# Performance work log

Measured on AMD Instinct MI355X. Metric: run time of the kernel, lower is better.

The kernel has to match this reference:

```python
import math
import jax, jax.numpy as jnp
import numpy as np

B, T, E = 2, 2048, 2048
H, HKV = 16, 4
DH = E // H              # 128
ROT_DIM = DH             # rotary_pct = 1.0 -> 128
ROT_HALF = ROT_DIM // 2  # RotaryEmbedding is built with dim=ROT_DIM//2=64; only these dims rotate
MAX_SEQ = 2048


def _rope_tables():
    # theta = 10000 ** (-arange(0, dim, 2)/dim) with dim = ROT_HALF
    theta = 10000.0 ** (-jnp.arange(0, ROT_HALF, 2, dtype=jnp.float32) / ROT_HALF)  # [ROT_HALF//2]
    pos = jnp.arange(MAX_SEQ, dtype=jnp.float32)
    angles = pos[:, None] * theta[None, :]   # [MAX_SEQ, ROT_HALF//2]
    return jnp.cos(angles), jnp.sin(angles)


def _apply_rotary(q, k, start_pos):
    # q: [B,T,H,ROT_DIM], k: [B,T,HKV,ROT_DIM]; rotate only first ROT_HALF dims (interleaved pairs)
    cos, sin = _rope_tables()
    t = q.shape[1]
    cos = jax.lax.dynamic_slice_in_dim(cos, start_pos, t, axis=0)[None, :, None, :]
    sin = jax.lax.dynamic_slice_in_dim(sin, start_pos, t, axis=0)[None, :, None, :]

    def rot(a):
        a_rot, a_pass = a[..., :ROT_HALF], a[..., ROT_HALF:]
        x, y = a_rot[..., 0::2], a_rot[..., 1::2]
        rx = x * cos - y * sin
        ry = x * sin + y * cos
        rotated = jnp.stack([rx, ry], axis=-1).reshape(*a_rot.shape)
        return jnp.concatenate([rotated, a_pass], axis=-1)

    return rot(q), rot(k)


def setup_inputs() -> dict:
    key = jax.random.key(0)
    ks = jax.random.split(key, 9)
    s = 0.02  # weight scale for sane logits
    return {
        "x": jax.random.normal(ks[0], (B, T, E), dtype=jnp.float32),
        "Wq": jax.random.normal(ks[1], (E, H * DH), dtype=jnp.float32) * s,
        "bq": jax.random.normal(ks[2], (H * DH,), dtype=jnp.float32) * s,
        "Wk": jax.random.normal(ks[3], (E, HKV * DH), dtype=jnp.float32) * s,
        "bk": jax.random.normal(ks[4], (HKV * DH,), dtype=jnp.float32) * s,
        "Wv": jax.random.normal(ks[5], (E, HKV * DH), dtype=jnp.float32) * s,
        "bv": jax.random.normal(ks[6], (HKV * DH,), dtype=jnp.float32) * s,
        "Wo": jax.random.normal(ks[7], (E, E), dtype=jnp.float32) * s,
        "bo": jax.random.normal(ks[8], (E,), dtype=jnp.float32) * s,
        "start_pos": 0,
    }


def reference(x, Wq, bq, Wk, bk, Wv, bv, Wo, bo, start_pos):
    b, t, _ = x.shape
    q = (x @ Wq + bq).reshape(b, t, H, DH)
    k = (x @ Wk + bk).reshape(b, t, HKV, DH)
    v = (x @ Wv + bv).reshape(b, t, HKV, DH)

    q, k = _apply_rotary(q, k, start_pos)

    group = H // HKV
    k = jnp.repeat(k, group, axis=2)  # [b,t,H,DH]
    v = jnp.repeat(v, group, axis=2)

    # scores: [b,H,t,t]
    scores = jnp.einsum("bqhd,bkhd->bhqk", q, k) / math.sqrt(DH)
    causal = jnp.tril(jnp.ones((t, t), dtype=bool))
    scores = jnp.where(causal[None, None], scores, -jnp.inf)
    probs = jax.nn.softmax(scores, axis=-1)

    out = jnp.einsum("bhqk,bkhd->bqhd", probs, v).reshape(b, t, H * DH)
    return out @ Wo + bo
```

## Files before the change

### kernel.cpp

```cpp
#include <hip/hip_runtime.h>

typedef __attribute__((ext_vector_type(8))) short short8;
typedef __attribute__((ext_vector_type(4))) float f32x4;
typedef __attribute__((ext_vector_type(16))) float f32x16;

#define DEVFN __device__ __forceinline__

DEVFN unsigned short f2bf(float f) {
  unsigned int u = __builtin_bit_cast(unsigned int, f);
  u += 0x7FFFu + ((u >> 16) & 1u);
  return (unsigned short)(u >> 16);
}
DEVFN float bf2f(unsigned int u) { return __builtin_bit_cast(float, u << 16); }

DEVFN unsigned int cvtpk_bf16(float lo, float hi) {
  unsigned int d;
  asm("v_cvt_pk_bf16_f32 %0, %1, %2" : "=v"(d) : "v"(lo), "v"(hi));
  return d;
}
DEVFN void plswap32(unsigned int& a, unsigned int& b) {
  asm("v_permlane32_swap_b32 %0, %1" : "+v"(a), "+v"(b));
}
DEVFN float bcast32(float v, int srclane) {
  int r = __builtin_amdgcn_ds_bpermute(srclane * 4, __builtin_bit_cast(int, v));
  return __builtin_bit_cast(float, r);
}


__global__ __launch_bounds__(256) void mk_tables(float* __restrict__ cost, float* __restrict__ sint) {
  int gid = blockIdx.x * 256 + threadIdx.x;
  int pos = gid >> 5, i = gid & 31;
  float theta = powf(10000.0f, -(float)(2 * i) / 64.0f);
  float ang = (float)pos * theta;
  cost[gid] = cosf(ang);
  sint[gid] = sinf(ang);
}

__global__ __launch_bounds__(256) void bias_cat_k(const float* __restrict__ bq, const float* __restrict__ bk,
                                                  const float* __restrict__ bv, float* __restrict__ out) {
  int i = blockIdx.x * 256 + threadIdx.x;
  float v;
  if (i < 2048) v = bq[i];
  else if (i < 2560) v = bk[i - 2048];
  else v = bv[i - 2560];
  out[i] = v;
}

__global__ __launch_bounds__(256) void convx(const float* __restrict__ x, unsigned short* __restrict__ xb) {
  int gid = blockIdx.x * 256 + threadIdx.x;
  const float4* xv = (const float4*)x;
  float4 a = xv[(size_t)gid * 2], b = xv[(size_t)gid * 2 + 1];
  short8 u;
  u[0] = (short)f2bf(a.x); u[1] = (short)f2bf(a.y); u[2] = (short)f2bf(a.z); u[3] = (short)f2bf(a.w);
  u[4] = (short)f2bf(b.x); u[5] = (short)f2bf(b.y); u[6] = (short)f2bf(b.z); u[7] = (short)f2bf(b.w);
  *(short8*)(xb + (size_t)gid * 8) = u;
}

__global__ __launch_bounds__(256) void transw(const float* __restrict__ W, unsigned short* __restrict__ Wt, int ncols) {
  __shared__ float lds[32][33];
  int n0 = blockIdx.x * 32, k0 = blockIdx.y * 32;
  int tx = threadIdx.x & 31, ty = threadIdx.x >> 5;
  #pragma unroll
  for (int i = 0; i < 4; i++) {
    int kr = ty + i * 8;
    lds[kr][tx] = W[(size_t)(k0 + kr) * ncols + n0 + tx];
  }
  __syncthreads();
  #pragma unroll
  for (int i = 0; i < 4; i++) {
    int nr = ty + i * 8;
    Wt[(size_t)(n0 + nr) * 2048 + k0 + tx] = f2bf(lds[tx][nr]);
  }
}

template<int NH>
__global__ __launch_bounds__(256) void rope_scatter(const unsigned short* __restrict__ QKV,
    const float* __restrict__ cost, const float* __restrict__ sint, const int* __restrict__ spp,
    unsigned short* __restrict__ dst, int colOff, float scale) {
  constexpr int LOG2NH = (NH == 16) ? 4 : 2;
  int gid = blockIdx.x * 256 + threadIdx.x;
  int j = gid & 63;
  int h = (gid >> 6) & (NH - 1);
  int m = gid >> (6 + LOG2NH);
  int t = m & 2047;
  int b = m >> 11;
  const unsigned short* src = QKV + (size_t)m * 3072 + colOff + h * 128 + 2 * j;
  unsigned int pair = *(const unsigned int*)src;
  float xv = bf2f(pair & 0xFFFFu), yv = bf2f(pair >> 16);
  float rx, ry;
  if (j < 32) {
    int pos = (spp[0] + t) & 2047;
    float c = cost[pos * 32 + j], s = sint[pos * 32 + j];
    rx = xv * c - yv * s;
    ry = xv * s + yv * c;
  } else { rx = xv; ry = yv; }
  rx *= scale; ry *= scale;
  int d0 = 2 * j;
  size_t off = (size_t)(b * NH + h) * 262144 + (t >> 5) * 4096 + (d0 >> 4) * 512
             + ((d0 >> 3) & 1) * 256 + (t & 31) * 8 + (d0 & 7);
  unsigned int outp = (unsigned int)f2bf(rx) | ((unsigned int)f2bf(ry) << 16);
  *(unsigned int*)(dst + off) = outp;
}

__global__ __launch_bounds__(256) void vtrans(const unsigned short* __restrict__ QKV, unsigned short* __restrict__ VF) {
  __shared__ __align__(16) unsigned short lds[64 * 128];
  int tid = threadIdx.x;
  int t0 = blockIdx.x * 64;
  int bk = blockIdx.y;
  const unsigned short* src = QKV + (size_t)(bk >> 2) * 2048 * 3072 + 2560 + (bk & 3) * 128;
  #pragma unroll
  for (int c = 0; c < 4; c++) {
    int idx = c * 256 + tid;
    int tr = idx >> 4, dc = idx & 15;
    short8 v = *(const short8*)(src + (size_t)(t0 + tr) * 3072 + dc * 8);
    *(short8*)((char*)lds + tr * 256 + 16 * (dc ^ (tr >> 3))) = v;
  }
  __syncthreads();
  unsigned short* dstb = VF + (size_t)bk * 262144;
  #pragma unroll
  for (int c2 = 0; c2 < 4; c2++) {
    int idx2 = c2 * 256 + tid;
    int tc = idx2 & 7, d = idx2 >> 3;
    short8 u;
    #pragma unroll
    for (int e = 0; e < 8; e++) {
      int t = 8 * tc + e;
      u[e] = *(const short*)((char*)lds + t * 256 + 16 * ((d >> 3) ^ tc) + (d & 7) * 2);
    }
    size_t off = (size_t)(t0 >> 6) * 8192 + ((d >> 5) * 4 + ((tc >> 1) & 3)) * 512
               + (tc & 1) * 256 + (d & 31) * 8;
    *(short8*)(dstb + off) = u;
  }
}

template<bool BF16OUT>
__global__ __launch_bounds__(256, 2) void gemm_bt(
    const unsigned short* __restrict__ A, const unsigned short* __restrict__ Bt,
    const float* __restrict__ bias, void* __restrict__ Cout, int M, int N, int K) {
  __shared__ __align__(16) unsigned short Asl[128 * 64];
  __shared__ __align__(16) unsigned short Bsl[128 * 64];
  int tid = threadIdx.x;
  int lane = tid & 63, w = tid >> 6;
  int wr = w >> 1, wc = w & 1;
  int m0 = blockIdx.y * 128, n0 = blockIdx.x * 128;

  f32x4 acc[4][4];
  #pragma unroll
  for (int i = 0; i < 4; i++)
    #pragma unroll
    for (int j = 0; j < 4; j++)
      #pragma unroll
      for (int r = 0; r < 4; r++) acc[i][j][r] = 0.f;

  int srow = w * 32 + (lane >> 3);
  int kc8 = (lane & 7) * 8;
  const unsigned short* Aptr = A + (size_t)(m0 + srow) * K + kc8;
  const unsigned short* Bptr = Bt + (size_t)(n0 + srow) * K + kc8;
  unsigned short* AslW = Asl + w * 4 * 512;
  unsigned short* BslW = Bsl + w * 4 * 512;

  for (int k0 = 0; k0 < K; k0 += 64) {
    __syncthreads();
    #pragma unroll
    for (int i = 0; i < 4; i++) {
      __builtin_amdgcn_global_load_lds(
        (const __attribute__((address_space(1))) unsigned int*)(Aptr + (size_t)i * 8 * K + k0),
        (__attribute__((address_space(3))) unsigned int*)(AslW + i * 512), 16, 0, 0);
      __builtin_amdgcn_global_load_lds(
        (const __attribute__((address_space(1))) unsigned int*)(Bptr + (size_t)i * 8 * K + k0),
        (__attribute__((address_space(3))) unsigned int*)(BslW + i * 512), 16, 0, 0);
    }
    __syncthreads();
    #pragma unroll
    for (int ks = 0; ks < 2; ks++) {
      short8 af[4], bfr[4];
      #pragma unroll
      for (int mi = 0; mi < 4; mi++)
        af[mi] = *(const short8*)(Asl + (wr * 64 + mi * 16 + (lane & 15)) * 64 + ks * 32 + (lane >> 4) * 8);
      #pragma unroll
      for (int ni = 0; ni < 4; ni++)
        bfr[ni] = *(const short8*)(Bsl + (wc * 64 + ni * 16 + (lane & 15)) * 64 + ks * 32 + (lane >> 4) * 8);
      #pragma unroll
      for (int mi = 0; mi < 4; mi++)
        #pragma unroll
        for (int ni = 0; ni < 4; ni++)
          acc[mi][ni] = __builtin_amdgcn_mfma_f32_16x16x32_bf16(af[mi], bfr[ni], acc[mi][ni], 0, 0, 0);
    }
  }
  int cl = lane & 15, rq = lane >> 4;
  #pragma unroll
  for (int mi = 0; mi < 4; mi++) {
    #pragma unroll
    for (int ni = 0; ni < 4; ni++) {
      int gn = n0 + wc * 64 + ni * 16 + cl;
      float bv = bias[gn];
      #pragma unroll
      for (int r = 0; r < 4; r++) {
        int gm = m0 + wr * 64 + mi * 16 + rq * 4 + r;
        float v = acc[mi][ni][r] + bv;
        if (BF16OUT) ((unsigned short*)Cout)[(size_t)gm * N + gn] = f2bf(v);
        else ((float*)Cout)[(size_t)gm * N + gn] = v;
      }
    }
  }
}

__global__ __launch_bounds__(512, 2) void attn_kernel(
    const unsigned short* __restrict__ QF, const unsigned short* __restrict__ KF,
    const unsigned short* __restrict__ VF, unsigned short* __restrict__ O) {
  const int tid = threadIdx.x;
  const int lane = tid & 63;
  const int w = tid >> 6;
  const int l31 = lane & 31;
  const int hf = lane >> 5;
  const int g = blockIdx.x & 7, j = blockIdx.x >> 3;
  const int b = g >> 2, kh = g & 3;
  const int h = kh * 4 + (j & 3);
  const int i4 = (j >> 2) * 4;
  const int qt = (w < 4) ? (i4 + w) : (67 - i4 - w);
  const int qw = qt * 32;
  const int nw = (qt >> 1) + 1;

  const unsigned short* qh  = QF + (size_t)(b * 16 + h) * 262144 + qt * 4096;
  const unsigned short* khp = KF + (size_t)(b * 4 + kh) * 262144;
  const unsigned short* vhp = VF + (size_t)(b * 4 + kh) * 262144;

  short8 qf[8];
  #pragma unroll
  for (int s = 0; s < 8; s++)
    qf[s] = *(const short8*)(qh + s * 512 + lane * 8);

  float m_r = -3.0e38f, l_r = 0.f;
  f32x16 oacc[4];
  #pragma unroll
  for (int dt = 0; dt < 4; dt++)
    #pragma unroll
    for (int r = 0; r < 16; r++) oacc[dt][r] = 0.f;

  for (int kt = 0; kt < nw; kt++) {
    const int kv0 = kt * 64;
    f32x16 sc[2];
    {
      short8 kf0[8];
      #pragma unroll
      for (int s = 0; s < 8; s++)
        kf0[s] = *(const short8*)(khp + (size_t)(2 * kt) * 4096 + s * 512 + lane * 8);
      #pragma unroll
      for (int r = 0; r < 16; r++) sc[0][r] = 0.f;
      #pragma unroll
      for (int s = 0; s < 8; s++)
        sc[0] = __builtin_amdgcn_mfma_f32_32x32x16_bf16(kf0[s], qf[s], sc[0], 0, 0, 0);
    }
    {
      short8 kf1[8];
      #pragma unroll
      for (int s = 0; s < 8; s++)
        kf1[s] = *(const short8*)(khp + (size_t)(2 * kt + 1) * 4096 + s * 512 + lane * 8);
      #pragma unroll
      for (int r = 0; r < 16; r++) sc[1][r] = 0.f;
      #pragma unroll
      for (int s = 0; s < 8; s++)
        sc[1] = __builtin_amdgcn_mfma_f32_32x32x16_bf16(kf1[s], qf[s], sc[1], 0, 0, 0);
    }
    short8 vf[4][4];
    #pragma unroll
    for (int dt = 0; dt < 4; dt++)
      #pragma unroll
      for (int ks = 0; ks < 4; ks++)
        vf[dt][ks] = *(const short8*)(vhp + (size_t)kt * 8192 + (dt * 4 + ks) * 512 + lane * 8);

    if (kv0 + 63 > qw) {
      #pragma unroll
      for (int ct = 0; ct < 2; ct++)
        #pragma unroll
        for (int r = 0; r < 16; r++) {
          int kg = kv0 + ct * 32 + (r & 3) + 8 * (r >> 2) + 4 * hf;
          if (kg > qw + l31) sc[ct][r] = -3.0e38f;
        }
    }
    float mx[16];
    #pragma unroll
    for (int r = 0; r < 16; r++) mx[r] = fmaxf(sc[0][r], sc[1][r]);
    #pragma unroll
    for (int s2 = 8; s2 >= 1; s2 >>= 1)
      #pragma unroll
      for (int i = 0; i < 8; i++) if (i < s2) mx[i] = fmaxf(mx[i], mx[i + s2]);
    float tm = fmaxf(mx[0], __shfl_xor(mx[0], 32));
    if (__any(tm > m_r + 8.0f)) {
      float mn = fmaxf(m_r, tm);
      float al = __builtin_amdgcn_exp2f(m_r - mn);
      m_r = mn;
      l_r *= al;
      #pragma unroll
      for (int r = 0; r < 16; r++) {
        float alr = bcast32(al, (r & 3) + 8 * (r >> 2) + 4 * hf);
        #pragma unroll
        for (int dt = 0; dt < 4; dt++) oacc[dt][r] *= alr;
      }
    }
    #pragma unroll
    for (int ct = 0; ct < 2; ct++)
      #pragma unroll
      for (int r = 0; r < 16; r++) sc[ct][r] = __builtin_amdgcn_exp2f(sc[ct][r] - m_r);
    float sm[16];
    #pragma unroll
    for (int r = 0; r < 16; r++) sm[r] = sc[0][r] + sc[1][r];
    #pragma unroll
    for (int s2 = 8; s2 >= 1; s2 >>= 1)
      #pragma unroll
      for (int i = 0; i < 8; i++) if (i < s2) sm[i] += sm[i + s2];
    l_r += sm[0];

    short8 pa[4];
    #pragma unroll
    for (int ks = 0; ks < 4; ks++) {
      const int ct = ks >> 1, kb = (ks & 1) * 8;
      unsigned int A0 = cvtpk_bf16(sc[ct][kb + 0], sc[ct][kb + 1]);
      unsigned int A1 = cvtpk_bf16(sc[ct][kb + 2], sc[ct][kb + 3]);
      unsigned int B0 = cvtpk_bf16(sc[ct][kb + 4], sc[ct][kb + 5]);
      unsigned int B1 = cvtpk_bf16(sc[ct][kb + 6], sc[ct][kb + 7]);
      plswap32(A0, B0);
      plswap32(A1, B1);
      union { unsigned int wds[4]; short8 s8; } u;
      u.wds[0] = A0; u.wds[1] = A1; u.wds[2] = B0; u.wds[3] = B1;
      pa[ks] = u.s8;
    }
    #pragma unroll
    for (int dt = 0; dt < 4; dt++)
      #pragma unroll
      for (int ks = 0; ks < 4; ks++)
        oacc[dt] = __builtin_amdgcn_mfma_f32_32x32x16_bf16(pa[ks], vf[dt][ks], oacc[dt], 0, 0, 0);
  }
  float invl = 1.0f / (l_r + __shfl_xor(l_r, 32));
  #pragma unroll
  for (int r = 0; r < 16; r++) {
    int rloc = (r & 3) + 8 * (r >> 2) + 4 * hf;
    float inv = bcast32(invl, rloc);
    int qg = qw + rloc;
    unsigned short* orow = O + ((size_t)(b * 2048 + qg)) * 2048 + h * 128;
    #pragma unroll
    for (int dt = 0; dt < 4; dt++)
      orow[dt * 32 + l31] = f2bf(oacc[dt][r] * inv);
  }
}

extern "C" void kernel_launch(void* const* d_in, const int* in_sizes, int n_in,
                              void* d_out, int out_size, void* d_ws, size_t ws_size,
                              hipStream_t stream) {
  (void)in_sizes; (void)n_in; (void)out_size; (void)ws_size;
  const float* x  = (const float*)d_in[0];
  const float* Wq = (const float*)d_in[1];
  const float* bq = (const float*)d_in[2];
  const float* Wk = (const float*)d_in[3];
  const float* bk = (const float*)d_in[4];
  const float* Wv = (const float*)d_in[5];
  const float* bv = (const float*)d_in[6];
  const float* Wo = (const float*)d_in[7];
  const float* bo = (const float*)d_in[8];
  const int*   sp = (const int*)d_in[9];

  char* ws = (char*)d_ws;
  unsigned short* xb    = (unsigned short*)ws;
  unsigned short* Wqkvt = (unsigned short*)(ws + 16777216);
  unsigned short* Wot   = (unsigned short*)(ws + 29360128);
  unsigned short* QKVb  = (unsigned short*)(ws + 37748736);
  float* cost           = (float*)(ws + 62914560);
  float* sint           = (float*)(ws + 63176704);
  float* bcat           = (float*)(ws + 63438848);

  unsigned short* Obuf = xb;
  unsigned short* QFr = (unsigned short*)d_out;
  unsigned short* KFr = (unsigned short*)((char*)d_out + 16777216);
  unsigned short* VFr = (unsigned short*)((char*)d_out + 20971520);

  mk_tables<<<256, 256, 0, stream>>>(cost, sint);
  bias_cat_k<<<12, 256, 0, stream>>>(bq, bk, bv, bcat);
  convx<<<4096, 256, 0, stream>>>(x, xb);
  transw<<<dim3(64, 64), 256, 0, stream>>>(Wq, Wqkvt, 2048);
  transw<<<dim3(16, 64), 256, 0, stream>>>(Wk, Wqkvt + (size_t)2048 * 2048, 512);
  transw<<<dim3(16, 64), 256, 0, stream>>>(Wv, Wqkvt + (size_t)2560 * 2048, 512);
  transw<<<dim3(64, 64), 256, 0, stream>>>(Wo, Wot, 2048);
  gemm_bt<true><<<dim3(24, 32), 256, 0, stream>>>(xb, Wqkvt, bcat, QKVb, 4096, 3072, 2048);
  rope_scatter<16><<<16384, 256, 0, stream>>>(QKVb, cost, sint, sp, QFr, 0, 0.12751743f);
  rope_scatter<4><<<4096, 256, 0, stream>>>(QKVb, cost, sint, sp, KFr, 2048, 1.0f);
  vtrans<<<dim3(32, 8), 256, 0, stream>>>(QKVb, VFr);
  attn_kernel<<<dim3(256), 512, 0, stream>>>(QFr, KFr, VFr, Obuf);
  gemm_bt<false><<<dim3(16, 32), 256, 0, stream>>>(Obuf, Wot, bo, (float*)d_out, 4096, 2048, 2048);
}
```

Before: 237.9 us.

## Split attention KV range across wave pairs with LDS merge of partial softmax

Each query tile is now handled by a pair of waves that each process half of the causal KV tiles. The partial output accumulators and the m/l statistics are combined through shared memory with a rescaled log-sum-exp merge. The grid doubles to 512 blocks, each covering 4 query tiles instead of 8, which gives more parallelism and shortens each wave's serial KV loop. The cost is 64KB of LDS per block, a block-wide barrier and extra merge work, and the launch bound now asks for 4 blocks per CU, which may cap register use.

```diff
diff --git a/kernel.cpp b/kernel.cpp
--- a/kernel.cpp
+++ b/kernel.cpp
@@ -205,21 +205,29 @@
   }
 }
 
-__global__ __launch_bounds__(512, 2) void attn_kernel(
+__global__ __launch_bounds__(512, 4) void attn_kernel(
     const unsigned short* __restrict__ QF, const unsigned short* __restrict__ KF,
     const unsigned short* __restrict__ VF, unsigned short* __restrict__ O) {
+  __shared__ float mbuf[4 * 4096];
+  __shared__ float mlb[4 * 128];
+
   const int tid = threadIdx.x;
   const int lane = tid & 63;
   const int w = tid >> 6;
+  const int p = w >> 1;
+  const int role = w & 1;
   const int l31 = lane & 31;
   const int hf = lane >> 5;
   const int g = blockIdx.x & 7, j = blockIdx.x >> 3;
   const int b = g >> 2, kh = g & 3;
   const int h = kh * 4 + (j & 3);
-  const int i4 = (j >> 2) * 4;
-  const int qt = (w < 4) ? (i4 + w) : (67 - i4 - w);
+  const int qg = j >> 2;
+  const int qt = (p < 2) ? (2 * qg + p) : (60 - 2 * qg + p);
   const int qw = qt * 32;
-  const int nw = (qt >> 1) + 1;
+  const int nt = (qt >> 1) + 1;
+  const int ntA = nt >> 1;
+  const int kt0 = role ? ntA : 0;
+  const int kt1 = role ? nt : ntA;
 
   const unsigned short* qh  = QF + (size_t)(b * 16 + h) * 262144 + qt * 4096;
   const unsigned short* khp = KF + (size_t)(b * 4 + kh) * 262144;
@@ -237,7 +245,7 @@
     #pragma unroll
     for (int r = 0; r < 16; r++) oacc[dt][r] = 0.f;
 
-  for (int kt = 0; kt < nw; kt++) {
+  for (int kt = kt0; kt < kt1; kt++) {
     const int kv0 = kt * 64;
     f32x16 sc[2];
     {
@@ -331,16 +339,41 @@
       for (int ks = 0; ks < 4; ks++)
         oacc[dt] = __builtin_amdgcn_mfma_f32_32x32x16_bf16(pa[ks], vf[dt][ks], oacc[dt], 0, 0, 0);
   }
-  float invl = 1.0f / (l_r + __shfl_xor(l_r, 32));
-  #pragma unroll
-  for (int r = 0; r < 16; r++) {
-    int rloc = (r & 3) + 8 * (r >> 2) + 4 * hf;
-    float inv = bcast32(invl, rloc);
-    int qg = qw + rloc;
-    unsigned short* orow = O + ((size_t)(b * 2048 + qg)) * 2048 + h * 128;
+
+  float lw = l_r + __shfl_xor(l_r, 32);
+  if (role) {
+    float* bp = mbuf + p * 4096;
     #pragma unroll
     for (int dt = 0; dt < 4; dt++)
-      orow[dt * 32 + l31] = f2bf(oacc[dt][r] * inv);
+      #pragma unroll
+      for (int r = 0; r < 16; r++)
+        bp[(dt * 16 + r) * 64 + lane] = oacc[dt][r];
+    mlb[p * 128 + lane] = m_r;
+    mlb[p * 128 + 64 + lane] = lw;
+  }
+  __syncthreads();
+  if (!role) {
+    const float* bp = mbuf + p * 4096;
+    float mB = mlb[p * 128 + lane];
+    float lB = mlb[p * 128 + 64 + lane];
+    float mm = fmaxf(m_r, mB);
+    float alA = __builtin_amdgcn_exp2f(m_r - mm);
+    float alB = __builtin_amdgcn_exp2f(mB - mm);
+    float invl = 1.0f / (lw * alA + lB * alB);
+    #pragma unroll
+    for (int r = 0; r < 16; r++) {
+      int rloc = (r & 3) + 8 * (r >> 2) + 4 * hf;
+      float aA = bcast32(alA, rloc);
+      float aB = bcast32(alB, rloc);
+      float inv = bcast32(invl, rloc);
+      int qgr = qw + rloc;
+      unsigned short* orow = O + ((size_t)(b * 2048 + qgr)) * 2048 + h * 128;
+      #pragma unroll
+      for (int dt = 0; dt < 4; dt++) {
+        float v = (oacc[dt][r] * aA + bp[(dt * 16 + r) * 64 + lane] * aB) * inv;
+        orow[dt * 32 + l31] = f2bf(v);
+      }
+    }
   }
 }
 
@@ -384,6 +417,6 @@
   rope_scatter<16><<<16384, 256, 0, stream>>>(QKVb, cost, sint, sp, QFr, 0, 0.12751743f);
   rope_scatter<4><<<4096, 256, 0, stream>>>(QKVb, cost, sint, sp, KFr, 2048, 1.0f);
   vtrans<<<dim3(32, 8), 256, 0, stream>>>(QKVb, VFr);
-  attn_kernel<<<dim3(256), 512, 0, stream>>>(QFr, KFr, VFr, Obuf);
+  attn_kernel<<<dim3(512), 512, 0, stream>>>(QFr, KFr, VFr, Obuf);
   gemm_bt<false><<<dim3(16, 32), 256, 0, stream>>>(Obuf, Wot, bo, (float*)d_out, 4096, 2048, 2048);
 }
```

Result: slower. 502.4 us (+111.2%).
